# Performance work log

Measured on AMD Instinct MI355X. Metric: run time of the kernel, lower is better.

Reference implementation:

```python
import jax, jax.numpy as jnp
import numpy as np

V, D, DFF, E, K, L = 32000, 1024, 4096, 8, 2, 2
B, S = 2, 1024


def _layer_norm(x, scale, bias, eps=1e-5):
    mu = jnp.mean(x, axis=-1, keepdims=True)
    var = jnp.var(x, axis=-1, keepdims=True)
    return (x - mu) * jax.lax.rsqrt(var + eps) * scale + bias


def setup_inputs() -> dict:
    key = jax.random.key(0)
    ks = jax.random.split(key, 16)
    s = 0.02
    return {
        "input_ids": jax.random.randint(ks[0], (B, S), 0, V, dtype=jnp.int32),
        "emb": jax.random.normal(ks[1], (V, D), jnp.float32) * s,
        "t_ln_scale": jnp.ones((L, D), jnp.float32),
        "t_ln_bias": jnp.zeros((L, D), jnp.float32),
        "t_w1": jax.random.normal(ks[2], (L, D, DFF), jnp.float32) * s,
        "t_b1": jnp.zeros((L, DFF), jnp.float32),
        "t_w2": jax.random.normal(ks[3], (L, DFF, D), jnp.float32) * s,
        "t_b2": jnp.zeros((L, D), jnp.float32),
        "Wr": jax.random.normal(ks[4], (D, E), jnp.float32) * s,
        "br": jnp.zeros((E,), jnp.float32),
        "e_w1": jax.random.normal(ks[5], (E, D, DFF), jnp.float32) * s,
        "e_b1": jnp.zeros((E, DFF), jnp.float32),
        "e_w2": jax.random.normal(ks[6], (E, DFF, D), jnp.float32) * s,
        "e_b2": jnp.zeros((E, D), jnp.float32),
        "Wl": jax.random.normal(ks[7], (D, V), jnp.float32) * s,
        "bl": jnp.zeros((V,), jnp.float32),
    }


def reference(input_ids, emb, t_ln_scale, t_ln_bias, t_w1, t_b1, t_w2, t_b2,
              Wr, br, e_w1, e_b1, e_w2, e_b2, Wl, bl):
    # token embeddings: [B,S,D]
    x = emb[input_ids]

    # temporal abstraction: L pre-LN residual MLP blocks
    for l in range(L):
        h = _layer_norm(x, t_ln_scale[l], t_ln_bias[l])
        h = jax.nn.gelu(jnp.einsum('bsd,df->bsf', h, t_w1[l]) + t_b1[l])
        x = x + jnp.einsum('bsf,fd->bsd', h, t_w2[l]) + t_b2[l]

    # router: top-k renormalized softmax over experts, scattered to [B,S,E]
    r_logits = jnp.einsum('bsd,de->bse', x, Wr) + br
    top_vals, top_idx = jax.lax.top_k(r_logits, K)
    top_w = jax.nn.softmax(top_vals, axis=-1)
    routing_weights = jnp.put_along_axis(
        jnp.zeros_like(r_logits), top_idx, top_w, axis=-1, inplace=False)

    # dense all-experts stack: [B,S,E,D]
    h = jax.nn.gelu(jnp.einsum('bsd,edf->bsef', x, e_w1) + e_b1)
    expert_out = jnp.einsum('bsef,efd->bsed', h, e_w2) + e_b2

    # sparse-weighted combine
    y = jnp.einsum('bse,bsed->bsd', routing_weights, expert_out)

    logits = jnp.einsum('bsd,dv->bsv', y, Wl) + bl
    return logits, routing_weights
```

## Files before the change

### kernel.cpp

```cpp
#include <hip/hip_runtime.h>
#include <stdint.h>

typedef __bf16 bf16;
typedef __bf16 bf16x8 __attribute__((ext_vector_type(8)));
typedef float f32x4 __attribute__((ext_vector_type(4)));

#define DEV __device__ __forceinline__

static constexpr int Dm   = 1024;
static constexpr int DFFm = 4096;
static constexpr int Tm   = 2048;
static constexpr int Vm   = 32000;

#define GLOAD_LDS16(g, l)                                                      \
  __builtin_amdgcn_global_load_lds(                                            \
      (const __attribute__((address_space(1))) unsigned int*)(g),              \
      (__attribute__((address_space(3))) unsigned int*)(l), 16, 0, 0)

DEV float gelu_tanh(float v) {
  float u = 0.7978845608028654f * (v + 0.044715f * v * v * v);
  float e = __expf(2.0f * u);
  float t = 1.0f - 2.0f / (e + 1.0f);
  return 0.5f * v * (1.0f + t);
}

template <bool SWZ>
__launch_bounds__(512, 2)
__global__ void gemm256_8p(const bf16* __restrict__ A, const bf16* __restrict__ B,
                           const float* __restrict__ bias, float* __restrict__ out,
                           int Kc, int Nc) {
  __shared__ bf16 lds[65536];
  const int tid  = threadIdx.x;
  const int lane = tid & 63;
  const int wid  = tid >> 6;
  const int wr   = wid >> 2;
  const int wc   = wid & 3;

  int bx = blockIdx.x, by = blockIdx.y;
  if constexpr (SWZ) {
    const int gx = gridDim.x, gy = gridDim.y;
    const int nwg = gx * gy;
    const int lin = by * gx + bx;
    const int q = nwg >> 3, r = nwg & 7;
    const int xcd = lin & 7, loc = lin >> 3;
    const int nid = (xcd < r ? xcd * (q + 1) : r * (q + 1) + (xcd - r) * q) + loc;
    bx = nid / gy; by = nid % gy;
  }
  const long am0 = (long)by * 256;
  const long bn0 = (long)bx * 256;
  const long K = Kc;
  const int NT = Kc >> 6;

  const int sub = (lane & 7) ^ (lane >> 3);
  const int rw  = wid * 8 + (lane >> 3);
  const bf16 *aS[4], *bS[4];
#pragma unroll
  for (int j = 0; j < 4; ++j) {
    aS[j] = A + (am0 + j * 64 + rw) * K + sub * 8;
    bS[j] = B + (bn0 + j * 64 + rw) * K + sub * 8;
  }
  char* ldsc = (char*)(void*)lds;

#define STG_A(kt, j)                                                           \
  GLOAD_LDS16(aS[j] + (long)(kt) * 64,                                         \
              ldsc + ((kt) & 1) * 65536 + ((j) * 64 + wid * 8) * 128)
#define STG_B(kt, j)                                                           \
  GLOAD_LDS16(bS[j] + (long)(kt) * 64,                                         \
              ldsc + ((kt) & 1) * 65536 + 32768 + ((j) * 64 + wid * 8) * 128)

  STG_B(0, 0); STG_B(0, 1); STG_B(0, 2); STG_B(0, 3);
  STG_A(0, 0); STG_A(0, 2); STG_A(0, 1); STG_A(0, 3);
  if (NT > 1) {
    STG_B(1, 0); STG_B(1, 1); STG_B(1, 2); STG_B(1, 3);
    STG_A(1, 0); STG_A(1, 2);
    asm volatile("s_waitcnt vmcnt(6)" ::: "memory");
  } else {
    asm volatile("s_waitcnt vmcnt(0)" ::: "memory");
  }
  __builtin_amdgcn_s_barrier();

  f32x4 acc[8][4] = {};
  const int r15 = lane & 15;
  const int kcs = lane >> 4;
  const int x7  = lane & 7;
  const int q80 = (kcs ^ x7) << 3;
  const int q81 = ((kcs + 4) ^ x7) << 3;

  for (int t = 0; t < NT; ++t) {
    const bf16* LAb = lds + (t & 1) * 32768 + wr * 128 * 64;
    const bf16* LBb = lds + (t & 1) * 32768 + 16384 + wc * 64 * 64;
    bf16x8 b0[4], b1[4];

    {
      bf16x8 a0, a1, a2, a3;
#pragma unroll
      for (int n = 0; n < 4; ++n) {
        b0[n] = *(const bf16x8*)(LBb + (n * 16 + r15) * 64 + q80);
        b1[n] = *(const bf16x8*)(LBb + (n * 16 + r15) * 64 + q81);
      }
      a0 = *(const bf16x8*)(LAb + (0 * 16 + r15) * 64 + q80);
      a1 = *(const bf16x8*)(LAb + (0 * 16 + r15) * 64 + q81);
      a2 = *(const bf16x8*)(LAb + (1 * 16 + r15) * 64 + q80);
      a3 = *(const bf16x8*)(LAb + (1 * 16 + r15) * 64 + q81);
      if (t + 1 < NT) { STG_A(t + 1, 1); STG_A(t + 1, 3); }
      __builtin_amdgcn_s_barrier();
      asm volatile("s_waitcnt lgkmcnt(0)" ::: "memory");
      __builtin_amdgcn_s_setprio(1);
#pragma unroll
      for (int n = 0; n < 4; ++n) {
        acc[0][n] = __builtin_amdgcn_mfma_f32_16x16x32_bf16(a0, b0[n], acc[0][n], 0, 0, 0);
        acc[0][n] = __builtin_amdgcn_mfma_f32_16x16x32_bf16(a1, b1[n], acc[0][n], 0, 0, 0);
        acc[1][n] = __builtin_amdgcn_mfma_f32_16x16x32_bf16(a2, b0[n], acc[1][n], 0, 0, 0);
        acc[1][n] = __builtin_amdgcn_mfma_f32_16x16x32_bf16(a3, b1[n], acc[1][n], 0, 0, 0);
      }
      __builtin_amdgcn_s_setprio(0);
      __builtin_amdgcn_s_barrier();
    }
    {
      bf16x8 a0, a1, a2, a3;
      a0 = *(const bf16x8*)(LAb + (2 * 16 + r15) * 64 + q80);
      a1 = *(const bf16x8*)(LAb + (2 * 16 + r15) * 64 + q81);
      a2 = *(const bf16x8*)(LAb + (3 * 16 + r15) * 64 + q80);
      a3 = *(const bf16x8*)(LAb + (3 * 16 + r15) * 64 + q81);
      if (t + 2 < NT) { STG_B(t + 2, 0); STG_B(t + 2, 1); }
      __builtin_amdgcn_s_barrier();
      asm volatile("s_waitcnt lgkmcnt(0)" ::: "memory");
      __builtin_amdgcn_s_setprio(1);
#pragma unroll
      for (int n = 0; n < 4; ++n) {
        acc[2][n] = __builtin_amdgcn_mfma_f32_16x16x32_bf16(a0, b0[n], acc[2][n], 0, 0, 0);
        acc[2][n] = __builtin_amdgcn_mfma_f32_16x16x32_bf16(a1, b1[n], acc[2][n], 0, 0, 0);
        acc[3][n] = __builtin_amdgcn_mfma_f32_16x16x32_bf16(a2, b0[n], acc[3][n], 0, 0, 0);
        acc[3][n] = __builtin_amdgcn_mfma_f32_16x16x32_bf16(a3, b1[n], acc[3][n], 0, 0, 0);
      }
      __builtin_amdgcn_s_setprio(0);
      __builtin_amdgcn_s_barrier();
    }
    {
      bf16x8 a0, a1, a2, a3;
      a0 = *(const bf16x8*)(LAb + (4 * 16 + r15) * 64 + q80);
      a1 = *(const bf16x8*)(LAb + (4 * 16 + r15) * 64 + q81);
      a2 = *(const bf16x8*)(LAb + (5 * 16 + r15) * 64 + q80);
      a3 = *(const bf16x8*)(LAb + (5 * 16 + r15) * 64 + q81);
      if (t + 2 < NT) { STG_B(t + 2, 2); STG_B(t + 2, 3); }
      __builtin_amdgcn_s_barrier();
      asm volatile("s_waitcnt lgkmcnt(0)" ::: "memory");
      __builtin_amdgcn_s_setprio(1);
#pragma unroll
      for (int n = 0; n < 4; ++n) {
        acc[4][n] = __builtin_amdgcn_mfma_f32_16x16x32_bf16(a0, b0[n], acc[4][n], 0, 0, 0);
        acc[4][n] = __builtin_amdgcn_mfma_f32_16x16x32_bf16(a1, b1[n], acc[4][n], 0, 0, 0);
        acc[5][n] = __builtin_amdgcn_mfma_f32_16x16x32_bf16(a2, b0[n], acc[5][n], 0, 0, 0);
        acc[5][n] = __builtin_amdgcn_mfma_f32_16x16x32_bf16(a3, b1[n], acc[5][n], 0, 0, 0);
      }
      __builtin_amdgcn_s_setprio(0);
      __builtin_amdgcn_s_barrier();
    }
    {
      bf16x8 a0, a1, a2, a3;
      a0 = *(const bf16x8*)(LAb + (6 * 16 + r15) * 64 + q80);
      a1 = *(const bf16x8*)(LAb + (6 * 16 + r15) * 64 + q81);
      a2 = *(const bf16x8*)(LAb + (7 * 16 + r15) * 64 + q80);
      a3 = *(const bf16x8*)(LAb + (7 * 16 + r15) * 64 + q81);
      if (t + 2 < NT) {
        STG_A(t + 2, 0); STG_A(t + 2, 2);
        asm volatile("s_waitcnt vmcnt(6)" ::: "memory");
      } else if (t + 1 < NT) {
        asm volatile("s_waitcnt vmcnt(0)" ::: "memory");
      }
      __builtin_amdgcn_s_barrier();
      asm volatile("s_waitcnt lgkmcnt(0)" ::: "memory");
      __builtin_amdgcn_s_setprio(1);
#pragma unroll
      for (int n = 0; n < 4; ++n) {
        acc[6][n] = __builtin_amdgcn_mfma_f32_16x16x32_bf16(a0, b0[n], acc[6][n], 0, 0, 0);
        acc[6][n] = __builtin_amdgcn_mfma_f32_16x16x32_bf16(a1, b1[n], acc[6][n], 0, 0, 0);
        acc[7][n] = __builtin_amdgcn_mfma_f32_16x16x32_bf16(a2, b0[n], acc[7][n], 0, 0, 0);
        acc[7][n] = __builtin_amdgcn_mfma_f32_16x16x32_bf16(a3, b1[n], acc[7][n], 0, 0, 0);
      }
      __builtin_amdgcn_s_setprio(0);
      __builtin_amdgcn_s_barrier();
    }
  }
#undef STG_A
#undef STG_B

  const long N = Nc;
#pragma unroll
  for (int m = 0; m < 8; ++m) {
#pragma unroll
    for (int n = 0; n < 4; ++n) {
      const long col = bn0 + wc * 64 + n * 16 + r15;
      const float bv = bias[col];
#pragma unroll
      for (int r = 0; r < 4; ++r) {
        const long row = am0 + wr * 128 + m * 16 + (lane >> 4) * 4 + r;
        out[row * N + col] = acc[m][n][r] + bv;
      }
    }
  }
}

enum { EPI_GELU_SPLIT = 0, EPI_RESID = 1, EPI_GELU_BF16 = 2, EPI_MOE = 3 };

struct GemmP {
  const bf16* Ah;
  const bf16* Bh;
  const float* bias;
  const float* rwp;
  const int* cnt;
  const int* idx;
  float* outF;
  bf16* outH;
  int K; int N;
  int lda; int ldb; int ldo;
  long aBS, bBS, outBS;
  int biasBS;
  int ebase;
  int kcShift; int kcK;
};

template <int EPI, bool GATHER, bool SWZ>
__launch_bounds__(256, 2)
__global__ void gemm_bt(GemmP p) {
  __shared__ bf16 lds[16384];
  bf16* ldsA = lds;
  bf16* ldsB = lds + 8192;

  const int tid  = threadIdx.x;
  const int lane = tid & 63;
  const int wid  = tid >> 6;
  const int wr   = wid >> 1;
  const int wc   = wid & 1;
  const int z    = blockIdx.z;
  const int kc   = z & ((1 << p.kcShift) - 1);
  const int ze   = z >> p.kcShift;

  int bx = blockIdx.x, by = blockIdx.y;
  if constexpr (SWZ) {
    const int gx = gridDim.x, gy = gridDim.y;
    const int nwg = gx * gy;
    const int lin = by * gx + bx;
    const int q = nwg >> 3, r = nwg & 7;
    const int xcd = lin & 7, loc = lin >> 3;
    const int nid = (xcd < r ? xcd * (q + 1) : r * (q + 1) + (xcd - r) * q) + loc;
    bx = nid / gy; by = nid % gy;
  }

  const long am0 = (long)by * 128;
  const long bn0 = (long)bx * 128;

  int cntE = 0;
  const int* il = nullptr;
  if constexpr (GATHER || EPI == EPI_MOE) {
    cntE = p.cnt[p.ebase + ze];
    if (am0 >= cntE) return;
    il = p.idx + (long)(p.ebase + ze) * 2048;
  }

  const long lda = p.lda, ldb = p.ldb;
  const long K = p.K;
  const long kco = (long)kc * p.kcK;

  const int sub = (lane & 7) ^ (lane >> 3);
  const int rIn = wid * 8 + (lane >> 3);

  const bf16 *aS[4], *bS[4];
  {
    const bf16* Bb = p.Bh + (long)ze * p.bBS + kco + bn0 * ldb;
    const bf16* Ab = p.Ah + (long)ze * p.aBS + kco + am0 * lda;
#pragma unroll
    for (int j = 0; j < 4; ++j) {
      const int row = j * 32 + rIn;
      bS[j] = Bb + (long)row * ldb + sub * 8;
      if constexpr (GATHER) {
        const int rt = (int)am0 + row;
        const long grow = il[rt < cntE ? rt : 0];
        aS[j] = p.Ah + grow * lda + kco + sub * 8;
      } else {
        aS[j] = Ab + (long)row * lda + sub * 8;
      }
    }
  }
  char* dstA[4];
#pragma unroll
  for (int j = 0; j < 4; ++j)
    dstA[j] = (char*)(void*)lds + (j * 256 + wid * 64) * 16;

  f32x4 acc[4][4] = {};

  const int r15 = lane & 15;
  const int kcs = lane >> 4;
  const int xk  = lane & 7;

  for (long k0 = 0; k0 < K; k0 += 64) {
    __syncthreads();
#pragma unroll
    for (int j = 0; j < 4; ++j) {
      GLOAD_LDS16(aS[j] + k0, dstA[j]);
      GLOAD_LDS16(bS[j] + k0, dstA[j] + 16384);
    }
    __syncthreads();
#pragma unroll
    for (int h = 0; h < 2; ++h) {
      const int q8 = ((kcs + 4 * h) ^ xk) << 3;
      bf16x8 a[4], b[4];
#pragma unroll
      for (int m = 0; m < 4; ++m)
        a[m] = *(const bf16x8*)(ldsA + (wr * 64 + m * 16 + r15) * 64 + q8);
#pragma unroll
      for (int n = 0; n < 4; ++n)
        b[n] = *(const bf16x8*)(ldsB + (wc * 64 + n * 16 + r15) * 64 + q8);
#pragma unroll
      for (int m = 0; m < 4; ++m)
#pragma unroll
        for (int n = 0; n < 4; ++n)
          acc[m][n] = __builtin_amdgcn_mfma_f32_16x16x32_bf16(a[m], b[n], acc[m][n], 0, 0, 0);
    }
  }

  const long N = p.N;
#pragma unroll
  for (int m = 0; m < 4; ++m) {
#pragma unroll
    for (int n = 0; n < 4; ++n) {
      const long col = bn0 + wc * 64 + n * 16 + (lane & 15);
      const float bv = (kc == 0) ? p.bias[(long)ze * p.biasBS + col] : 0.0f;
#pragma unroll
      for (int r = 0; r < 4; ++r) {
        const long row = am0 + wr * 64 + m * 16 + (lane >> 4) * 4 + r;
        float v = acc[m][n][r] + bv;
        if constexpr (EPI == EPI_GELU_SPLIT) {
          float g = gelu_tanh(v);
          bf16 hh = (bf16)g;
          long o = row * (long)p.ldo + col;
          p.outH[o] = hh;
          p.outH[o + N] = (bf16)(g - (float)hh);
          p.outH[o + 2 * N] = hh;
        } else if constexpr (EPI == EPI_RESID) {
          atomicAdd(p.outF + row * N + col, v);
        } else if constexpr (EPI == EPI_GELU_BF16) {
          long o = (long)ze * p.outBS + row * N + col;
          p.outH[o] = (bf16)gelu_tanh(v);
        } else if constexpr (EPI == EPI_MOE) {
          if (row < cntE) {
            const int tok = il[row];
            const float wgt = p.rwp[(long)tok * 8 + p.ebase + ze];
            atomicAdd(p.outF + (long)tok * N + col, wgt * v);
          }
        }
      }
    }
  }
}

template <bool AUG>
__global__ void transpose_cvt(const float* __restrict__ in, bf16* __restrict__ out,
                              int R, int C, long inBS, long outBS) {
  __shared__ float tile[32][33];
  const float* inp = in + (long)blockIdx.z * inBS;
  const long c0 = (long)blockIdx.x * 32;
  const long r0 = (long)blockIdx.y * 32;
  const int tx = threadIdx.x;
  const int ty = threadIdx.y;
#pragma unroll
  for (int i = 0; i < 4; ++i) {
    int r = ty + i * 8;
    tile[r][tx] = inp[(r0 + r) * (long)C + c0 + tx];
  }
  __syncthreads();
  const long ob = (long)blockIdx.z * outBS;
  const long stride = AUG ? 3L * R : (long)R;
#pragma unroll
  for (int i = 0; i < 4; ++i) {
    int c = ty + i * 8;
    float v = tile[tx][c];
    bf16 h = (bf16)v;
    long o = ob + (c0 + c) * stride + r0 + tx;
    out[o] = h;
    if constexpr (AUG) {
      out[o + R] = h;
      out[o + 2 * R] = (bf16)(v - (float)h);
    }
  }
}

__global__ void embed_kernel(const int* __restrict__ ids, const float* __restrict__ emb,
                             float* __restrict__ x) {
  const long t = blockIdx.x;
  const int id = ids[t];
  ((float4*)(x + t * 1024))[threadIdx.x] = ((const float4*)(emb + (long)id * 1024))[threadIdx.x];
}

__global__ void ln_aug_kernel(const float* __restrict__ x, const float* __restrict__ sc,
                              const float* __restrict__ bi, bf16* __restrict__ oa) {
  const long t = blockIdx.x;
  const int tid = threadIdx.x;
  const int lane = tid & 63, wid = tid >> 6;
  float4 a = ((const float4*)(x + t * 1024))[tid];
  float s = a.x + a.y + a.z + a.w;
  float q = a.x * a.x + a.y * a.y + a.z * a.z + a.w * a.w;
#pragma unroll
  for (int off = 32; off; off >>= 1) {
    s += __shfl_down(s, off);
    q += __shfl_down(q, off);
  }
  __shared__ float sr[4], qr[4];
  if (lane == 0) { sr[wid] = s; qr[wid] = q; }
  __syncthreads();
  s = sr[0] + sr[1] + sr[2] + sr[3];
  q = qr[0] + qr[1] + qr[2] + qr[3];
  const float mu = s * (1.0f / 1024.0f);
  const float var = q * (1.0f / 1024.0f) - mu * mu;
  const float rs = rsqrtf(var + 1e-5f);
#pragma unroll
  for (int j = 0; j < 4; ++j) {
    const int d = tid * 4 + j;
    const float g = (((const float*)&a)[j] - mu) * rs * sc[d] + bi[d];
    const bf16 h = (bf16)g;
    oa[t * 3072 + d] = h;
    oa[t * 3072 + 1024 + d] = (bf16)(g - (float)h);
    oa[t * 3072 + 2048 + d] = h;
  }
}

__global__ void router_kernel(const float* __restrict__ x, const float* __restrict__ Wr,
                              const float* __restrict__ br, float* __restrict__ rwo,
                              int* __restrict__ top2) {
  const long t = blockIdx.x;
  const int lane = threadIdx.x;
  float acc[8];
#pragma unroll
  for (int e = 0; e < 8; ++e) acc[e] = 0.0f;
  const float4* xr = (const float4*)(x + t * 1024);
#pragma unroll
  for (int j = 0; j < 4; ++j) {
    const int d4 = j * 64 + lane;
    float4 xv = xr[d4];
#pragma unroll
    for (int u = 0; u < 4; ++u) {
      const float xs = ((const float*)&xv)[u];
      const float4* wp = (const float4*)(Wr + (long)(d4 * 4 + u) * 8);
      float4 w0 = wp[0], w1 = wp[1];
      acc[0] += xs * w0.x; acc[1] += xs * w0.y; acc[2] += xs * w0.z; acc[3] += xs * w0.w;
      acc[4] += xs * w1.x; acc[5] += xs * w1.y; acc[6] += xs * w1.z; acc[7] += xs * w1.w;
    }
  }
#pragma unroll
  for (int off = 32; off; off >>= 1)
#pragma unroll
    for (int e = 0; e < 8; ++e) acc[e] += __shfl_down(acc[e], off);
  if (lane == 0) {
    float v[8];
#pragma unroll
    for (int e = 0; e < 8; ++e) v[e] = acc[e] + br[e];
    int i0 = 0; float v0 = v[0];
    for (int e = 1; e < 8; ++e) if (v[e] > v0) { v0 = v[e]; i0 = e; }
    int i1 = -1; float v1 = -3.4e38f;
    for (int e = 0; e < 8; ++e) if (e != i0 && v[e] > v1) { v1 = v[e]; i1 = e; }
    float e1 = expf(v1 - v0);
    float den = 1.0f + e1;
    float w0 = 1.0f / den, w1 = e1 / den;
    float* o = rwo + t * 8;
#pragma unroll
    for (int e = 0; e < 8; ++e) o[e] = (e == i0) ? w0 : (e == i1 ? w1 : 0.0f);
    top2[t] = i0 | (i1 << 8);
  }
}

__global__ void build_lists(const int* __restrict__ top2, int* __restrict__ cnt,
                            int* __restrict__ idx) {
  const int t = blockIdx.x * 256 + threadIdx.x;
  const int rec = top2[t];
  const int e0 = rec & 255, e1 = (rec >> 8) & 255;
  int p0 = atomicAdd(&cnt[e0], 1);
  idx[e0 * 2048 + p0] = t;
  int p1 = atomicAdd(&cnt[e1], 1);
  idx[e1 * 2048 + p1] = t;
}

__global__ void cvt_bf16_kernel(const float* __restrict__ in, bf16* __restrict__ out, long n) {
  long i = ((long)blockIdx.x * blockDim.x + threadIdx.x) * 8;
  if (i >= n) return;
  float4 a = *(const float4*)(in + i);
  float4 b = *(const float4*)(in + i + 4);
  bf16x8 o;
  o[0] = (bf16)a.x; o[1] = (bf16)a.y; o[2] = (bf16)a.z; o[3] = (bf16)a.w;
  o[4] = (bf16)b.x; o[5] = (bf16)b.y; o[6] = (bf16)b.z; o[7] = (bf16)b.w;
  *(bf16x8*)(out + i) = o;
}

extern "C" void kernel_launch(void* const* d_in, const int* in_sizes, int n_in,
                              void* d_out, int out_size, void* d_ws, size_t ws_size,
                              hipStream_t stream) {
  (void)in_sizes; (void)n_in; (void)out_size; (void)ws_size;
  const int*   ids  = (const int*)d_in[0];
  const float* emb  = (const float*)d_in[1];
  const float* tlns = (const float*)d_in[2];
  const float* tlnb = (const float*)d_in[3];
  const float* tw1  = (const float*)d_in[4];
  const float* tb1  = (const float*)d_in[5];
  const float* tw2  = (const float*)d_in[6];
  const float* tb2  = (const float*)d_in[7];
  const float* Wr   = (const float*)d_in[8];
  const float* br   = (const float*)d_in[9];
  const float* ew1  = (const float*)d_in[10];
  const float* eb1  = (const float*)d_in[11];
  const float* ew2  = (const float*)d_in[12];
  const float* eb2  = (const float*)d_in[13];
  const float* Wl   = (const float*)d_in[14];
  const float* bl   = (const float*)d_in[15];

  float* logits = (float*)d_out;
  float* rwout  = (float*)d_out + (long)Tm * Vm;

  size_t off = 0;
  auto take = [&](size_t bytes) {
    void* pp = (char*)d_ws + off;
    off += (bytes + 255) & ~(size_t)255;
    return pp;
  };
  float* X    = (float*)take((size_t)Tm * Dm * 4);
  bf16*  XB   = (bf16*) take((size_t)Tm * Dm * 2);
  float* Y    = (float*)take((size_t)Tm * Dm * 4);
  bf16*  YB   = (bf16*) take((size_t)Tm * Dm * 2);
  int*   top2 = (int*)  take((size_t)Tm * 4);
  int*   cnt  = (int*)  take(8 * 4);
  int*   idxl = (int*)  take((size_t)8 * Tm * 4);
  char*  S    = (char*) take(134217728);

  bf16* A1  = (bf16*)S;
  bf16* W1A = (bf16*)(S + 12582912);
  bf16* W2A = (bf16*)(S + 12582912 + 25165824);
  bf16* HTA = (bf16*)(S + 12582912 + 2 * 25165824);
  bf16* EW1T = (bf16*)S;
  bf16* HE   = (bf16*)(S + 33554432);
  bf16* EW2T = (bf16*)(S + 100663296);
  bf16* WLT  = (bf16*)S;

  embed_kernel<<<dim3(Tm), dim3(256), 0, stream>>>(ids, emb, X);

  for (int l = 0; l < 2; ++l) {
    transpose_cvt<true><<<dim3(DFFm / 32, Dm / 32, 1), dim3(32, 8), 0, stream>>>(
        tw1 + (long)l * Dm * DFFm, W1A, Dm, DFFm, 0, 0);
    transpose_cvt<true><<<dim3(Dm / 32, DFFm / 32, 1), dim3(32, 8), 0, stream>>>(
        tw2 + (long)l * DFFm * Dm, W2A, DFFm, Dm, 0, 0);
    ln_aug_kernel<<<dim3(Tm), dim3(256), 0, stream>>>(X, tlns + l * Dm, tlnb + l * Dm, A1);

    GemmP p1{};
    p1.Ah = A1; p1.Bh = W1A;
    p1.bias = tb1 + (long)l * DFFm;
    p1.outH = HTA;
    p1.K = 3072; p1.N = DFFm; p1.lda = 3072; p1.ldb = 3072; p1.ldo = 3 * DFFm;
    gemm_bt<EPI_GELU_SPLIT, false, true>
        <<<dim3(DFFm / 128, Tm / 128, 1), dim3(256), 0, stream>>>(p1);

    GemmP p2{};
    p2.Ah = HTA; p2.Bh = W2A;
    p2.bias = tb2 + (long)l * Dm;
    p2.outF = X;
    p2.K = 1536; p2.N = Dm; p2.lda = 12288; p2.ldb = 12288;
    p2.kcShift = 3; p2.kcK = 1536;
    gemm_bt<EPI_RESID, false, true>
        <<<dim3(Dm / 128, Tm / 128, 8), dim3(256), 0, stream>>>(p2);
  }

  router_kernel<<<dim3(Tm), dim3(64), 0, stream>>>(X, Wr, br, rwout, top2);
  hipMemsetAsync(cnt, 0, 8 * 4, stream);
  build_lists<<<dim3(Tm / 256), dim3(256), 0, stream>>>(top2, cnt, idxl);
  cvt_bf16_kernel<<<dim3(Tm * Dm / (256 * 8)), dim3(256), 0, stream>>>(X, XB, (long)Tm * Dm);
  hipMemsetAsync(Y, 0, (size_t)Tm * Dm * 4, stream);

  for (int q = 0; q < 2; ++q) {
    transpose_cvt<false><<<dim3(DFFm / 32, Dm / 32, 4), dim3(32, 8), 0, stream>>>(
        ew1 + (long)q * 4 * Dm * DFFm, EW1T, Dm, DFFm, (long)Dm * DFFm, (long)DFFm * Dm);
    transpose_cvt<false><<<dim3(Dm / 32, DFFm / 32, 4), dim3(32, 8), 0, stream>>>(
        ew2 + (long)q * 4 * DFFm * Dm, EW2T, DFFm, Dm, (long)DFFm * Dm, (long)Dm * DFFm);

    GemmP pe1{};
    pe1.Ah = XB; pe1.Bh = EW1T;
    pe1.bias = eb1 + (long)q * 4 * DFFm; pe1.biasBS = DFFm;
    pe1.outH = HE; pe1.outBS = (long)Tm * DFFm;
    pe1.aBS = 0; pe1.bBS = (long)DFFm * Dm;
    pe1.cnt = cnt; pe1.idx = idxl; pe1.ebase = q * 4;
    pe1.K = Dm; pe1.N = DFFm; pe1.lda = Dm; pe1.ldb = Dm;
    gemm_bt<EPI_GELU_BF16, true, true>
        <<<dim3(DFFm / 128, Tm / 128, 4), dim3(256), 0, stream>>>(pe1);

    GemmP pe2{};
    pe2.Ah = HE; pe2.aBS = (long)Tm * DFFm;
    pe2.Bh = EW2T; pe2.bBS = (long)Dm * DFFm;
    pe2.bias = eb2 + (long)q * 4 * Dm; pe2.biasBS = Dm;
    pe2.rwp = rwout; pe2.cnt = cnt; pe2.idx = idxl; pe2.ebase = q * 4;
    pe2.outF = Y;
    pe2.K = 1024; pe2.N = Dm; pe2.lda = DFFm; pe2.ldb = DFFm;
    pe2.kcShift = 2; pe2.kcK = 1024;
    gemm_bt<EPI_MOE, false, true>
        <<<dim3(Dm / 128, Tm / 128, 16), dim3(256), 0, stream>>>(pe2);
  }

  cvt_bf16_kernel<<<dim3(Tm * Dm / (256 * 8)), dim3(256), 0, stream>>>(Y, YB, (long)Tm * Dm);
  transpose_cvt<false><<<dim3(Vm / 32, Dm / 32, 1), dim3(32, 8), 0, stream>>>(
      Wl, WLT, Dm, Vm, 0, 0);
  gemm256_8p<true><<<dim3(Vm / 256, Tm / 256, 1), dim3(512), 0, stream>>>(
      YB, WLT, bl, logits, Dm, Vm);
}
```

Baseline: 979.7 us.

## Compact split-bf16 operands to two copies, vectorize transposes, fuse router bookkeeping

```diff
diff --git a/kernel.cpp b/kernel.cpp
--- a/kernel.cpp
+++ b/kernel.cpp
@@ -3,6 +3,7 @@
 
 typedef __bf16 bf16;
 typedef __bf16 bf16x8 __attribute__((ext_vector_type(8)));
+typedef __bf16 bf16x4 __attribute__((ext_vector_type(4)));
 typedef float f32x4 __attribute__((ext_vector_type(4)));
 
 #define DEV __device__ __forceinline__
@@ -218,6 +219,7 @@
   int biasBS;
   int ebase;
   int kcShift; int kcK;
+  int aT, aS2, bT, bS2;
 };
 
 template <int EPI, bool GATHER, bool SWZ>
@@ -267,8 +269,8 @@
 
   const bf16 *aS[4], *bS[4];
   {
-    const bf16* Bb = p.Bh + (long)ze * p.bBS + kco + bn0 * ldb;
-    const bf16* Ab = p.Ah + (long)ze * p.aBS + kco + am0 * lda;
+    const bf16* Bb = p.Bh + (long)ze * p.bBS + bn0 * ldb;
+    const bf16* Ab = p.Ah + (long)ze * p.aBS + am0 * lda;
 #pragma unroll
     for (int j = 0; j < 4; ++j) {
       const int row = j * 32 + rIn;
@@ -276,7 +278,7 @@
       if constexpr (GATHER) {
         const int rt = (int)am0 + row;
         const long grow = il[rt < cntE ? rt : 0];
-        aS[j] = p.Ah + grow * lda + kco + sub * 8;
+        aS[j] = p.Ah + grow * lda + sub * 8;
       } else {
         aS[j] = Ab + (long)row * lda + sub * 8;
       }
@@ -294,11 +296,14 @@
   const int xk  = lane & 7;
 
   for (long k0 = 0; k0 < K; k0 += 64) {
+    const long kv = kco + k0;
+    const long ka = (kv >= p.aT) ? kv - p.aS2 : kv;
+    const long kb = (kv >= p.bT) ? kv - p.bS2 : kv;
     __syncthreads();
 #pragma unroll
     for (int j = 0; j < 4; ++j) {
-      GLOAD_LDS16(aS[j] + k0, dstA[j]);
-      GLOAD_LDS16(bS[j] + k0, dstA[j] + 16384);
+      GLOAD_LDS16(aS[j] + ka, dstA[j]);
+      GLOAD_LDS16(bS[j] + kb, dstA[j] + 16384);
     }
     __syncthreads();
 #pragma unroll
@@ -336,7 +341,6 @@
           long o = row * (long)p.ldo + col;
           p.outH[o] = hh;
           p.outH[o + N] = (bf16)(g - (float)hh);
-          p.outH[o + 2 * N] = hh;
         } else if constexpr (EPI == EPI_RESID) {
           atomicAdd(p.outF + row * N + col, v);
         } else if constexpr (EPI == EPI_GELU_BF16) {
@@ -357,31 +361,38 @@
 template <bool AUG>
 __global__ void transpose_cvt(const float* __restrict__ in, bf16* __restrict__ out,
                               int R, int C, long inBS, long outBS) {
-  __shared__ float tile[32][33];
+  __shared__ float tile[64][65];
   const float* inp = in + (long)blockIdx.z * inBS;
-  const long c0 = (long)blockIdx.x * 32;
-  const long r0 = (long)blockIdx.y * 32;
+  const long c0 = (long)blockIdx.x * 64;
+  const long r0 = (long)blockIdx.y * 64;
   const int tx = threadIdx.x;
   const int ty = threadIdx.y;
 #pragma unroll
   for (int i = 0; i < 4; ++i) {
-    int r = ty + i * 8;
-    tile[r][tx] = inp[(r0 + r) * (long)C + c0 + tx];
+    const int r = ty + i * 16;
+    const float4 v = *(const float4*)(inp + (r0 + r) * (long)C + c0 + tx * 4);
+    tile[r][tx * 4 + 0] = v.x;
+    tile[r][tx * 4 + 1] = v.y;
+    tile[r][tx * 4 + 2] = v.z;
+    tile[r][tx * 4 + 3] = v.w;
   }
   __syncthreads();
   const long ob = (long)blockIdx.z * outBS;
-  const long stride = AUG ? 3L * R : (long)R;
-#pragma unroll
-  for (int i = 0; i < 4; ++i) {
-    int c = ty + i * 8;
-    float v = tile[tx][c];
-    bf16 h = (bf16)v;
-    long o = ob + (c0 + c) * stride + r0 + tx;
-    out[o] = h;
-    if constexpr (AUG) {
-      out[o + R] = h;
-      out[o + 2 * R] = (bf16)(v - (float)h);
-    }
+  const long stride = AUG ? 2L * R : (long)R;
+#pragma unroll
+  for (int j = 0; j < 4; ++j) {
+    const int c = j * 16 + ty;
+    bf16x4 h, l;
+#pragma unroll
+    for (int u = 0; u < 4; ++u) {
+      float v = tile[tx * 4 + u][c];
+      bf16 hh = (bf16)v;
+      h[u] = hh;
+      if constexpr (AUG) l[u] = (bf16)(v - (float)hh);
+    }
+    const long o = ob + (c0 + c) * stride + r0 + tx * 4;
+    *(bf16x4*)(out + o) = h;
+    if constexpr (AUG) *(bf16x4*)(out + o + R) = l;
   }
 }
 
@@ -392,8 +403,8 @@
   ((float4*)(x + t * 1024))[threadIdx.x] = ((const float4*)(emb + (long)id * 1024))[threadIdx.x];
 }
 
-__global__ void ln_aug_kernel(const float* __restrict__ x, const float* __restrict__ sc,
-                              const float* __restrict__ bi, bf16* __restrict__ oa) {
+__global__ void ln_aug2_kernel(const float* __restrict__ x, const float* __restrict__ sc,
+                               const float* __restrict__ bi, bf16* __restrict__ oa) {
   const long t = blockIdx.x;
   const int tid = threadIdx.x;
   const int lane = tid & 63, wid = tid >> 6;
@@ -418,15 +429,15 @@
     const int d = tid * 4 + j;
     const float g = (((const float*)&a)[j] - mu) * rs * sc[d] + bi[d];
     const bf16 h = (bf16)g;
-    oa[t * 3072 + d] = h;
-    oa[t * 3072 + 1024 + d] = (bf16)(g - (float)h);
-    oa[t * 3072 + 2048 + d] = h;
+    oa[t * 2048 + d] = h;
+    oa[t * 2048 + 1024 + d] = (bf16)(g - (float)h);
   }
 }
 
 __global__ void router_kernel(const float* __restrict__ x, const float* __restrict__ Wr,
                               const float* __restrict__ br, float* __restrict__ rwo,
-                              int* __restrict__ top2) {
+                              bf16* __restrict__ xb, int* __restrict__ cnt,
+                              int* __restrict__ idx) {
   const long t = blockIdx.x;
   const int lane = threadIdx.x;
   float acc[8];
@@ -437,6 +448,9 @@
   for (int j = 0; j < 4; ++j) {
     const int d4 = j * 64 + lane;
     float4 xv = xr[d4];
+    bf16x4 xh;
+    xh[0] = (bf16)xv.x; xh[1] = (bf16)xv.y; xh[2] = (bf16)xv.z; xh[3] = (bf16)xv.w;
+    *(bf16x4*)(xb + t * 1024 + (long)d4 * 4) = xh;
 #pragma unroll
     for (int u = 0; u < 4; ++u) {
       const float xs = ((const float*)&xv)[u];
@@ -464,19 +478,11 @@
     float* o = rwo + t * 8;
 #pragma unroll
     for (int e = 0; e < 8; ++e) o[e] = (e == i0) ? w0 : (e == i1 ? w1 : 0.0f);
-    top2[t] = i0 | (i1 << 8);
-  }
-}
-
-__global__ void build_lists(const int* __restrict__ top2, int* __restrict__ cnt,
-                            int* __restrict__ idx) {
-  const int t = blockIdx.x * 256 + threadIdx.x;
-  const int rec = top2[t];
-  const int e0 = rec & 255, e1 = (rec >> 8) & 255;
-  int p0 = atomicAdd(&cnt[e0], 1);
-  idx[e0 * 2048 + p0] = t;
-  int p1 = atomicAdd(&cnt[e1], 1);
-  idx[e1 * 2048 + p1] = t;
+    int p0 = atomicAdd(&cnt[i0], 1);
+    idx[i0 * 2048 + p0] = (int)t;
+    int p1 = atomicAdd(&cnt[i1], 1);
+    idx[i1 * 2048 + p1] = (int)t;
+  }
 }
 
 __global__ void cvt_bf16_kernel(const float* __restrict__ in, bf16* __restrict__ out, long n) {
@@ -524,15 +530,14 @@
   bf16*  XB   = (bf16*) take((size_t)Tm * Dm * 2);
   float* Y    = (float*)take((size_t)Tm * Dm * 4);
   bf16*  YB   = (bf16*) take((size_t)Tm * Dm * 2);
-  int*   top2 = (int*)  take((size_t)Tm * 4);
   int*   cnt  = (int*)  take(8 * 4);
   int*   idxl = (int*)  take((size_t)8 * Tm * 4);
   char*  S    = (char*) take(134217728);
 
   bf16* A1  = (bf16*)S;
-  bf16* W1A = (bf16*)(S + 12582912);
-  bf16* W2A = (bf16*)(S + 12582912 + 25165824);
-  bf16* HTA = (bf16*)(S + 12582912 + 2 * 25165824);
+  bf16* W1A = (bf16*)(S + 8388608);
+  bf16* W2A = (bf16*)(S + 25165824);
+  bf16* HTA = (bf16*)(S + 41943040);
   bf16* EW1T = (bf16*)S;
   bf16* HE   = (bf16*)(S + 33554432);
   bf16* EW2T = (bf16*)(S + 100663296);
@@ -541,17 +546,18 @@
   embed_kernel<<<dim3(Tm), dim3(256), 0, stream>>>(ids, emb, X);
 
   for (int l = 0; l < 2; ++l) {
-    transpose_cvt<true><<<dim3(DFFm / 32, Dm / 32, 1), dim3(32, 8), 0, stream>>>(
+    transpose_cvt<true><<<dim3(DFFm / 64, Dm / 64, 1), dim3(16, 16), 0, stream>>>(
         tw1 + (long)l * Dm * DFFm, W1A, Dm, DFFm, 0, 0);
-    transpose_cvt<true><<<dim3(Dm / 32, DFFm / 32, 1), dim3(32, 8), 0, stream>>>(
+    transpose_cvt<true><<<dim3(Dm / 64, DFFm / 64, 1), dim3(16, 16), 0, stream>>>(
         tw2 + (long)l * DFFm * Dm, W2A, DFFm, Dm, 0, 0);
-    ln_aug_kernel<<<dim3(Tm), dim3(256), 0, stream>>>(X, tlns + l * Dm, tlnb + l * Dm, A1);
+    ln_aug2_kernel<<<dim3(Tm), dim3(256), 0, stream>>>(X, tlns + l * Dm, tlnb + l * Dm, A1);
 
     GemmP p1{};
     p1.Ah = A1; p1.Bh = W1A;
     p1.bias = tb1 + (long)l * DFFm;
     p1.outH = HTA;
-    p1.K = 3072; p1.N = DFFm; p1.lda = 3072; p1.ldb = 3072; p1.ldo = 3 * DFFm;
+    p1.K = 3072; p1.N = DFFm; p1.lda = 2048; p1.ldb = 2048; p1.ldo = 2 * DFFm;
+    p1.aT = 2048; p1.aS2 = 2048; p1.bT = 1024; p1.bS2 = 1024;
     gemm_bt<EPI_GELU_SPLIT, false, true>
         <<<dim3(DFFm / 128, Tm / 128, 1), dim3(256), 0, stream>>>(p1);
 
@@ -559,22 +565,21 @@
     p2.Ah = HTA; p2.Bh = W2A;
     p2.bias = tb2 + (long)l * Dm;
     p2.outF = X;
-    p2.K = 1536; p2.N = Dm; p2.lda = 12288; p2.ldb = 12288;
+    p2.K = 1536; p2.N = Dm; p2.lda = 8192; p2.ldb = 8192;
     p2.kcShift = 3; p2.kcK = 1536;
+    p2.aT = 8192; p2.aS2 = 8192; p2.bT = 4096; p2.bS2 = 4096;
     gemm_bt<EPI_RESID, false, true>
         <<<dim3(Dm / 128, Tm / 128, 8), dim3(256), 0, stream>>>(p2);
   }
 
-  router_kernel<<<dim3(Tm), dim3(64), 0, stream>>>(X, Wr, br, rwout, top2);
   hipMemsetAsync(cnt, 0, 8 * 4, stream);
-  build_lists<<<dim3(Tm / 256), dim3(256), 0, stream>>>(top2, cnt, idxl);
-  cvt_bf16_kernel<<<dim3(Tm * Dm / (256 * 8)), dim3(256), 0, stream>>>(X, XB, (long)Tm * Dm);
+  router_kernel<<<dim3(Tm), dim3(64), 0, stream>>>(X, Wr, br, rwout, XB, cnt, idxl);
   hipMemsetAsync(Y, 0, (size_t)Tm * Dm * 4, stream);
 
   for (int q = 0; q < 2; ++q) {
-    transpose_cvt<false><<<dim3(DFFm / 32, Dm / 32, 4), dim3(32, 8), 0, stream>>>(
+    transpose_cvt<false><<<dim3(DFFm / 64, Dm / 64, 4), dim3(16, 16), 0, stream>>>(
         ew1 + (long)q * 4 * Dm * DFFm, EW1T, Dm, DFFm, (long)Dm * DFFm, (long)DFFm * Dm);
-    transpose_cvt<false><<<dim3(Dm / 32, DFFm / 32, 4), dim3(32, 8), 0, stream>>>(
+    transpose_cvt<false><<<dim3(Dm / 64, DFFm / 64, 4), dim3(16, 16), 0, stream>>>(
         ew2 + (long)q * 4 * DFFm * Dm, EW2T, DFFm, Dm, (long)DFFm * Dm, (long)Dm * DFFm);
 
     GemmP pe1{};
@@ -600,7 +605,7 @@
   }
 
   cvt_bf16_kernel<<<dim3(Tm * Dm / (256 * 8)), dim3(256), 0, stream>>>(Y, YB, (long)Tm * Dm);
-  transpose_cvt<false><<<dim3(Vm / 32, Dm / 32, 1), dim3(32, 8), 0, stream>>>(
+  transpose_cvt<false><<<dim3(Vm / 64, Dm / 64, 1), dim3(16, 16), 0, stream>>>(
       Wl, WLT, Dm, Vm, 0, 0);
   gemm256_8p<true><<<dim3(Vm / 256, Tm / 256, 1), dim3(512), 0, stream>>>(
       YB, WLT, bl, logits, Dm, Vm);
```

After: 978.3 us (median of 2 runs). About the same (-0.1%).
